# Performance work log

Measured on AMD Instinct MI355X. Metric: run time of the kernel, lower is better.

Reference implementation:

```python
import jax, jax.numpy as jnp
import numpy as np

B, S, D, H, W = 2, 4096, 1024, 8, 1024  # batch, seq, model_dim, heads, window
DH = D // H
EPS = 1e-5


def setup_inputs() -> dict:
    key = jax.random.key(0)
    ks = jax.random.split(key, 4)
    scale = 0.02
    return {
        "val": jax.random.normal(ks[0], (B, S, D), dtype=jnp.float32),
        "w_qkv": jax.random.normal(ks[1], (D, 3 * D), dtype=jnp.float32) * scale,
        "b_qkv": jnp.zeros((3 * D,), dtype=jnp.float32),
        "w_out": jax.random.normal(ks[2], (D, D), dtype=jnp.float32) * scale,
        "b_out": jnp.zeros((D,), dtype=jnp.float32),
        "ln_gamma": jnp.ones((D,), dtype=jnp.float32),
        "ln_beta": jnp.zeros((D,), dtype=jnp.float32),
    }


def _layer_norm(x, gamma, beta):
    mu = jnp.mean(x, axis=-1, keepdims=True)
    var = jnp.mean(jnp.square(x - mu), axis=-1, keepdims=True)
    return (x - mu) * jax.lax.rsqrt(var + EPS) * gamma + beta


def reference(val, w_qkv, b_qkv, w_out, b_out, ln_gamma, ln_beta):
    nb = S // W  # number of local windows
    qkv = val @ w_qkv + b_qkv                       # [B, S, 3D]
    qkv = qkv.reshape(B, nb, W, 3, H, DH)
    q, k, v = qkv[..., 0, :, :], qkv[..., 1, :, :], qkv[..., 2, :, :]  # [B,nb,W,H,DH]
    scores = jnp.einsum("bnwhd,bnxhd->bnhwx", q, k) / jnp.sqrt(jnp.float32(DH))
    attn = jax.nn.softmax(scores, axis=-1)          # [B,nb,H,W,W]
    ctx = jnp.einsum("bnhwx,bnxhd->bnwhd", attn, v).reshape(B, S, D)
    attn_out = ctx @ w_out + b_out                  # [B,S,D]
    return _layer_norm(val + attn_out, ln_gamma, ln_beta)
```

## Files before the change

kernel.cpp:

```cpp
#include <hip/hip_runtime.h>
#include <hip/hip_bf16.h>
#include <stdint.h>


typedef float f32x4 __attribute__((ext_vector_type(4)));
typedef __bf16 bf16x8 __attribute__((ext_vector_type(8)));

static __device__ __forceinline__ unsigned short f2bf(float f) {
    unsigned int u = __builtin_bit_cast(unsigned int, f);
    u += 0x7fffu + ((u >> 16) & 1u);
    return (unsigned short)(u >> 16);
}

static __device__ __forceinline__ unsigned cvt_pk_bf16(float lo, float hi) {
    unsigned r;
    asm("v_cvt_pk_bf16_f32 %0, %1, %2" : "=v"(r) : "v"(lo), "v"(hi));
    return r;
}

static __device__ __forceinline__ void gload_lds16(const void* g, void* l) {
    __builtin_amdgcn_global_load_lds(
        (__attribute__((address_space(1))) void*)(g),
        (__attribute__((address_space(3))) void*)(l), 16, 0, 0);
}

#define VMCNT(n) asm volatile("s_waitcnt vmcnt(" #n ")" ::: "memory")
#define SB() __builtin_amdgcn_sched_barrier(0)

__global__ __launch_bounds__(256) void k_convert(const float* __restrict__ in,
                                                 unsigned short* __restrict__ out,
                                                 int n4) {
    int i = blockIdx.x * 256 + threadIdx.x;
    if (i >= n4) return;
    float4 v = ((const float4*)in)[i];
    ushort4 o;
    o.x = f2bf(v.x); o.y = f2bf(v.y); o.z = f2bf(v.z); o.w = f2bf(v.w);
    ((ushort4*)out)[i] = o;
}

__global__ __launch_bounds__(256) void k_transpose(const float* __restrict__ in,
                                                   unsigned short* __restrict__ out,
                                                   int R, int C) {
    __shared__ float tile[64][65];
    const int rt = blockIdx.y * 64, ct = blockIdx.x * 64;
    const int t = threadIdx.x;
#pragma unroll
    for (int i = 0; i < 4; ++i) {
        int fid = i * 256 + t;
        int r = fid >> 4;
        int c = (fid & 15) << 2;
        float4 v = *(const float4*)&in[(size_t)(rt + r) * C + ct + c];
        tile[r][c] = v.x; tile[r][c + 1] = v.y; tile[r][c + 2] = v.z; tile[r][c + 3] = v.w;
    }
    __syncthreads();
#pragma unroll
    for (int i = 0; i < 4; ++i) {
        int fid = i * 256 + t;
        int c = fid >> 4;
        int r0 = (fid & 15) << 2;
        ushort4 o;
        o.x = f2bf(tile[r0][c]);     o.y = f2bf(tile[r0 + 1][c]);
        o.z = f2bf(tile[r0 + 2][c]); o.w = f2bf(tile[r0 + 3][c]);
        *(ushort4*)&out[(size_t)(ct + c) * R + rt + r0] = o;
    }
}

template <int MODE, int NTILES>
__global__ __launch_bounds__(512) void k_gemm(
    const unsigned short* __restrict__ A,
    const unsigned short* __restrict__ Bt,
    const float* __restrict__ bias,
    const float* __restrict__ resid,
    unsigned short* __restrict__ out_qk,
    unsigned short* __restrict__ out_vT,
    float* __restrict__ out_f)
{
    __shared__ __align__(16) char smem[147456];
    const int t = threadIdx.x;
    const int wave = t >> 6, lane = t & 63;
    const int lr = lane & 15, lg = lane >> 4;
    const int wr = wave >> 1, wc = wave & 1;

    const int lid = blockIdx.x;
    const int swz = (lid & 7) * (4 * NTILES) + (lid >> 3);
    const int tile_m = (swz / NTILES) * 256;
    const int tile_n = (swz % NTILES) * 128;

    const int srow = lane >> 3;
    const int sblk = (lane & 7) ^ srow;

    f32x4 acc[4][4];
#pragma unroll
    for (int i = 0; i < 4; ++i)
#pragma unroll
        for (int j = 0; j < 4; ++j)
            acc[i][j] = (f32x4){0.f, 0.f, 0.f, 0.f};

    auto stage2 = [&](int kt, int buf, int h) {
#pragma unroll
        for (int i = 0; i < 2; ++i) {
            int r = h * 128 + i * 64 + wave * 8 + srow;
            int dst = buf * 49152 + h * 16384 + i * 8192 + wave * 1024 + lane * 16;
            gload_lds16(&A[(size_t)(tile_m + r) * 1024 + kt * 64 + sblk * 8], smem + dst);
        }
        int rb = h * 64 + wave * 8 + srow;
        int dstb = buf * 49152 + 32768 + h * 8192 + wave * 1024 + lane * 16;
        gload_lds16(&Bt[(size_t)(tile_n + rb) * 1024 + kt * 64 + sblk * 8], smem + dstb);
    };

    stage2(0, 0, 0); stage2(0, 0, 1);
    stage2(1, 1, 0); stage2(1, 1, 1);

    bf16x8 af[4][2], bf[2][2];

    for (int kt = 0; kt < 16; ++kt) {
        const int buf = kt % 3;
        if (kt == 15) { VMCNT(0); } else { VMCNT(6); }
        SB(); __builtin_amdgcn_s_barrier(); SB();

        if (kt < 14) {
            stage2(kt + 2, (kt + 2) % 3, 0);
            stage2(kt + 2, (kt + 2) % 3, 1);
        }

        const int abase = buf * 49152;
        const int bbase = buf * 49152 + 32768;

#pragma unroll
        for (int mi = 0; mi < 4; ++mi) {
            const int row = wr * 64 + mi * 16 + lr;
#pragma unroll
            for (int kk = 0; kk < 2; ++kk)
                af[mi][kk] = *(const bf16x8*)(smem + abase + row * 128 +
                                (((kk * 4 + lg) ^ (row & 7)) << 4));
        }
#pragma unroll
        for (int ni = 0; ni < 2; ++ni) {
            const int row = wc * 64 + ni * 16 + lr;
#pragma unroll
            for (int kk = 0; kk < 2; ++kk)
                bf[ni][kk] = *(const bf16x8*)(smem + bbase + row * 128 +
                                (((kk * 4 + lg) ^ (row & 7)) << 4));
        }

        __builtin_amdgcn_s_setprio(1);
#pragma unroll
        for (int kk = 0; kk < 2; ++kk)
#pragma unroll
            for (int mi = 0; mi < 4; ++mi)
#pragma unroll
                for (int ni = 0; ni < 2; ++ni)
                    acc[mi][ni] = __builtin_amdgcn_mfma_f32_16x16x32_bf16(
                        af[mi][kk], bf[ni][kk], acc[mi][ni], 0, 0, 0);
        __builtin_amdgcn_s_setprio(0);

#pragma unroll
        for (int ni = 0; ni < 2; ++ni) {
            const int row = wc * 64 + 32 + ni * 16 + lr;
#pragma unroll
            for (int kk = 0; kk < 2; ++kk)
                bf[ni][kk] = *(const bf16x8*)(smem + bbase + row * 128 +
                                (((kk * 4 + lg) ^ (row & 7)) << 4));
        }

        __builtin_amdgcn_s_setprio(1);
#pragma unroll
        for (int kk = 0; kk < 2; ++kk)
#pragma unroll
            for (int mi = 0; mi < 4; ++mi)
#pragma unroll
                for (int ni = 0; ni < 2; ++ni)
                    acc[mi][2 + ni] = __builtin_amdgcn_mfma_f32_16x16x32_bf16(
                        af[mi][kk], bf[ni][kk], acc[mi][2 + ni], 0, 0, 0);
        __builtin_amdgcn_s_setprio(0);
    }

#pragma unroll
    for (int J = 0; J < 4; ++J) {
        const int n = tile_n + wc * 64 + J * 16 + lr;
        const float bv = bias[n];
#pragma unroll
        for (int I = 0; I < 4; ++I) {
            const int m0 = tile_m + wr * 64 + I * 16 + lg * 4;
            f32x4 v = acc[I][J];
            if (MODE == 0) {
                if (n < 2048) {
#pragma unroll
                    for (int r = 0; r < 4; ++r)
                        out_qk[(size_t)(m0 + r) * 2048 + n] = f2bf(v[r] + bv);
                } else {
                    int hd = (n - 2048) >> 7;
                    int dd = (n - 2048) & 127;
                    int bn = m0 >> 10;
                    int x0 = m0 & 1023;
                    ushort4 o;
                    o.x = f2bf(v[0] + bv); o.y = f2bf(v[1] + bv);
                    o.z = f2bf(v[2] + bv); o.w = f2bf(v[3] + bv);
                    *(ushort4*)&out_vT[((size_t)(bn * 8 + hd) * 128 + dd) * 1024 + x0] = o;
                }
            } else {
#pragma unroll
                for (int r = 0; r < 4; ++r) {
                    size_t idx = (size_t)(m0 + r) * 1024 + n;
                    out_f[idx] = v[r] + bv + resid[idx];
                }
            }
        }
    }
}

__global__ __launch_bounds__(256, 2) void k_attn(
    const unsigned short* __restrict__ qk,
    const unsigned short* __restrict__ vT,
    unsigned short* __restrict__ ctx)
{
    __shared__ __align__(16) unsigned short Kl[2 * 64 * 128];
    __shared__ __align__(16) unsigned short Vl[2 * 128 * 64];
    __shared__ __align__(16) unsigned short Pl[128 * 64];
    const int t = threadIdx.x;
    const int wave = t >> 6, lane = t & 63;
    const int lr = lane & 15, lg = lane >> 4;

    const int lid = blockIdx.y * gridDim.x + blockIdx.x;
    const int xcd = lid & 7, slot = lid >> 3;
    const int head = xcd * 8 + (slot & 7);
    const int qblk = slot >> 3;

    const int h = head & 7;
    const int tok0 = (head >> 3) * 1024;
    const int qtok = tok0 + qblk * 128 + wave * 32;
    const float cl2 = 0.08838834764831845f * 1.44269504088896f;

    const unsigned short* kbase = &qk[(size_t)tok0 * 2048 + 1024 + h * 128];
    const unsigned short* vhead = &vT[(size_t)head * 128 * 1024];

    auto stage = [&](int x0, int buf) {
        unsigned short* Kb = (unsigned short*)((char*)Kl + buf * 16384);
        unsigned short* Vb = (unsigned short*)((char*)Vl + buf * 16384);
#pragma unroll
        for (int i = 0; i < 4; ++i) {
            int x = i * 16 + wave * 4 + (lane >> 4);
            int ck = (lane & 15) ^ (x & 7);
            gload_lds16(&kbase[(size_t)(x0 + x) * 2048 + ck * 8], &Kb[i * 2048 + wave * 512]);
            int d = i * 32 + wave * 8 + (lane >> 3);
            int cv = (lane & 7) ^ (d & 7);
            gload_lds16(&vhead[(size_t)d * 1024 + x0 + cv * 8], &Vb[i * 2048 + wave * 512]);
        }
    };

    bf16x8 qf[2][4];
#pragma unroll
    for (int nq = 0; nq < 2; ++nq)
#pragma unroll
        for (int kk = 0; kk < 4; ++kk)
            qf[nq][kk] = *(const bf16x8*)&qk[(size_t)(qtok + 16 * nq + lr) * 2048 + h * 128 + kk * 32 + lg * 8];

    f32x4 o[2][8];
#pragma unroll
    for (int a = 0; a < 2; ++a)
#pragma unroll
        for (int b = 0; b < 8; ++b)
            o[a][b] = (f32x4){0.f, 0.f, 0.f, 0.f};
    float m_run[2] = {-3.0e38f, -3.0e38f};
    float l_run[2] = {0.f, 0.f};

    stage(0, 0);

    for (int tile = 0; tile < 16; ++tile) {
        const int kb = (tile & 1) * 16384;
        if (tile < 15) {
            stage((tile + 1) * 64, (tile + 1) & 1);
            VMCNT(8);
        } else {
            VMCNT(0);
        }
        SB(); __builtin_amdgcn_s_barrier(); SB();

        f32x4 s[4][2];
#pragma unroll
        for (int mi = 0; mi < 4; ++mi)
#pragma unroll
            for (int nq = 0; nq < 2; ++nq)
                s[mi][nq] = (f32x4){0.f, 0.f, 0.f, 0.f};
#pragma unroll
        for (int kk = 0; kk < 4; ++kk) {
            bf16x8 kf[4];
#pragma unroll
            for (int mi = 0; mi < 4; ++mi) {
                int row = mi * 16 + lr;
                int byte = (row * 256 + kk * 64 + lg * 16) ^ ((row & 7) << 4);
                kf[mi] = *(const bf16x8*)((const char*)Kl + kb + byte);
            }
            __builtin_amdgcn_s_setprio(1);
#pragma unroll
            for (int mi = 0; mi < 4; ++mi)
#pragma unroll
                for (int nq = 0; nq < 2; ++nq)
                    s[mi][nq] = __builtin_amdgcn_mfma_f32_16x16x32_bf16(kf[mi], qf[nq][kk], s[mi][nq], 0, 0, 0);
            __builtin_amdgcn_s_setprio(0);
        }

        float fac[2];
        bool doresc[2];
#pragma unroll
        for (int nq = 0; nq < 2; ++nq) {
            float mx = -3.0e38f;
#pragma unroll
            for (int mi = 0; mi < 4; ++mi)
#pragma unroll
                for (int r = 0; r < 4; ++r)
                    mx = fmaxf(mx, s[mi][nq][r]);
            mx = fmaxf(mx, __shfl_xor(mx, 16));
            mx = fmaxf(mx, __shfl_xor(mx, 32));
            float mxl = mx * cl2;
            float mr = m_run[nq];
            if (__any(mxl - mr > 8.0f)) {
                float mn = fmaxf(mr, mxl);
                fac[nq] = __builtin_amdgcn_exp2f(mr - mn);
                m_run[nq] = mn;
                doresc[nq] = true;
            } else {
                fac[nq] = 1.0f;
                doresc[nq] = false;
            }
            const float nmn = -m_run[nq];
            float sum = 0.f;
            const int q = wave * 32 + nq * 16 + lr;
#pragma unroll
            for (int mi = 0; mi < 4; ++mi) {
                float p0 = __builtin_amdgcn_exp2f(__builtin_fmaf(s[mi][nq][0], cl2, nmn));
                float p1 = __builtin_amdgcn_exp2f(__builtin_fmaf(s[mi][nq][1], cl2, nmn));
                float p2 = __builtin_amdgcn_exp2f(__builtin_fmaf(s[mi][nq][2], cl2, nmn));
                float p3 = __builtin_amdgcn_exp2f(__builtin_fmaf(s[mi][nq][3], cl2, nmn));
                sum += (p0 + p1) + (p2 + p3);
                uint2 pk;
                pk.x = cvt_pk_bf16(p0, p1);
                pk.y = cvt_pk_bf16(p2, p3);
                int byte = (q * 128 + (mi * 16 + lg * 4) * 2) ^ ((q & 7) << 4);
                *(uint2*)((char*)Pl + byte) = pk;
            }
            sum += __shfl_xor(sum, 16);
            sum += __shfl_xor(sum, 32);
            l_run[nq] = l_run[nq] * fac[nq] + sum;
        }

#pragma unroll
        for (int mo = 0; mo < 2; ++mo)
            if (doresc[mo]) {
#pragma unroll
                for (int r = 0; r < 4; ++r) {
                    int src = (lane & 48) | (lg * 4 + r);
                    float f = __shfl(fac[mo], src);
#pragma unroll
                    for (int nd = 0; nd < 8; ++nd)
                        o[mo][nd][r] *= f;
                }
            }

#pragma unroll
        for (int kk = 0; kk < 2; ++kk) {
            bf16x8 pf[2], vf[8];
#pragma unroll
            for (int mo = 0; mo < 2; ++mo) {
                int q = wave * 32 + mo * 16 + lr;
                int byte = (q * 128 + kk * 64 + lg * 16) ^ ((q & 7) << 4);
                pf[mo] = *(const bf16x8*)((const char*)Pl + byte);
            }
#pragma unroll
            for (int nd = 0; nd < 8; ++nd) {
                int drow = nd * 16 + lr;
                int byte = (drow * 128 + kk * 64 + lg * 16) ^ ((drow & 7) << 4);
                vf[nd] = *(const bf16x8*)((const char*)Vl + kb + byte);
            }
            __builtin_amdgcn_s_setprio(1);
#pragma unroll
            for (int mo = 0; mo < 2; ++mo)
#pragma unroll
                for (int nd = 0; nd < 8; ++nd)
                    o[mo][nd] = __builtin_amdgcn_mfma_f32_16x16x32_bf16(pf[mo], vf[nd], o[mo][nd], 0, 0, 0);
            __builtin_amdgcn_s_setprio(0);
        }
        __builtin_amdgcn_s_barrier(); SB();
    }

#pragma unroll
    for (int mo = 0; mo < 2; ++mo) {
        float rl[4];
#pragma unroll
        for (int r = 0; r < 4; ++r) {
            int src = (lane & 48) | (lg * 4 + r);
            rl[r] = 1.0f / __shfl(l_run[mo], src);
        }
#pragma unroll
        for (int nd = 0; nd < 8; ++nd)
#pragma unroll
            for (int r = 0; r < 4; ++r) {
                int q = qtok + mo * 16 + lg * 4 + r;
                ctx[(size_t)q * 1024 + h * 128 + nd * 16 + lr] = f2bf(o[mo][nd][r] * rl[r]);
            }
    }
}

__global__ __launch_bounds__(256) void k_ln(float* __restrict__ io,
                                            const float* __restrict__ gamma,
                                            const float* __restrict__ beta)
{
    __shared__ float bs[4], bss[4];
    const int row = blockIdx.x;
    const int t = threadIdx.x;
    float4 v = ((const float4*)&io[(size_t)row * 1024])[t];
    float s = (v.x + v.y) + (v.z + v.w);
    float ss = (v.x * v.x + v.y * v.y) + (v.z * v.z + v.w * v.w);
#pragma unroll
    for (int off = 32; off >= 1; off >>= 1) {
        s += __shfl_xor(s, off);
        ss += __shfl_xor(ss, off);
    }
    if ((t & 63) == 0) { bs[t >> 6] = s; bss[t >> 6] = ss; }
    __syncthreads();
    s = (bs[0] + bs[1]) + (bs[2] + bs[3]);
    ss = (bss[0] + bss[1]) + (bss[2] + bss[3]);
    const float mu = s * (1.f / 1024.f);
    const float var = ss * (1.f / 1024.f) - mu * mu;
    const float rs = rsqrtf(var + 1e-5f);
    float4 g = ((const float4*)gamma)[t];
    float4 b = ((const float4*)beta)[t];
    float4 ov;
    ov.x = (v.x - mu) * rs * g.x + b.x;
    ov.y = (v.y - mu) * rs * g.y + b.y;
    ov.z = (v.z - mu) * rs * g.z + b.z;
    ov.w = (v.w - mu) * rs * g.w + b.w;
    ((float4*)&io[(size_t)row * 1024])[t] = ov;
}

extern "C" void kernel_launch(void* const* d_in, const int* in_sizes, int n_in,
                              void* d_out, int out_size, void* d_ws, size_t ws_size,
                              hipStream_t stream)
{
    const float* val   = (const float*)d_in[0];
    const float* w_qkv = (const float*)d_in[1];
    const float* b_qkv = (const float*)d_in[2];
    const float* w_out = (const float*)d_in[3];
    const float* b_out = (const float*)d_in[4];
    const float* ln_g  = (const float*)d_in[5];
    const float* ln_b  = (const float*)d_in[6];
    float* out = (float*)d_out;

    char* ws = (char*)d_ws;
    unsigned short* qk     = (unsigned short*)(ws + 0);
    unsigned short* vTb    = (unsigned short*)(ws + 33554432);
    unsigned short* ctx    = (unsigned short*)(ws + 50331648);
    unsigned short* w_outT = (unsigned short*)(ws + 67108864);
    unsigned short* w_qkvT = (unsigned short*)(ws + 69206016);
    unsigned short* valb   = (unsigned short*)(ws + 75497472);

    k_convert<<<8192, 256, 0, stream>>>(val, valb, 2097152);
    k_transpose<<<dim3(48, 16), 256, 0, stream>>>(w_qkv, w_qkvT, 1024, 3072);
    k_transpose<<<dim3(16, 16), 256, 0, stream>>>(w_out, w_outT, 1024, 1024);
    k_gemm<0, 24><<<768, 512, 0, stream>>>(valb, w_qkvT, b_qkv, nullptr, qk, vTb, nullptr);
    k_attn<<<dim3(8, 64), 256, 0, stream>>>(qk, vTb, ctx);
    k_gemm<1, 8><<<256, 512, 0, stream>>>(ctx, w_outT, b_out, val, nullptr, nullptr, out);
    k_ln<<<8192, 256, 0, stream>>>(out, ln_g, ln_b);
}
```

Before: 159.5 us.

## Halve GEMM block to 4 waves with 128x64 per-wave tiles

Rewrites the GEMM work split so each block runs 4 waves instead of 8, and each wave computes a 128x64 output sub-tile with 32 accumulators. Each wave now issues all of its staging loads and reuses A/B fragments across more MFMAs per LDS read, which cuts the number of LDS reads per MFMA. In exchange it roughly doubles accumulator register pressure (128 VGPRs for accumulators) and leaves fewer waves to hide latency.

```diff
diff --git a/kernel.cpp b/kernel.cpp
--- a/kernel.cpp
+++ b/kernel.cpp
@@ -66,7 +66,7 @@
 }
 
 template <int MODE, int NTILES>
-__global__ __launch_bounds__(512) void k_gemm(
+__global__ __launch_bounds__(256) void k_gemm(
     const unsigned short* __restrict__ A,
     const unsigned short* __restrict__ Bt,
     const float* __restrict__ bias,
@@ -89,90 +89,66 @@
     const int srow = lane >> 3;
     const int sblk = (lane & 7) ^ srow;
 
-    f32x4 acc[4][4];
-#pragma unroll
-    for (int i = 0; i < 4; ++i)
+    f32x4 acc[8][4];
+#pragma unroll
+    for (int i = 0; i < 8; ++i)
 #pragma unroll
         for (int j = 0; j < 4; ++j)
             acc[i][j] = (f32x4){0.f, 0.f, 0.f, 0.f};
 
-    auto stage2 = [&](int kt, int buf, int h) {
-#pragma unroll
-        for (int i = 0; i < 2; ++i) {
-            int r = h * 128 + i * 64 + wave * 8 + srow;
-            int dst = buf * 49152 + h * 16384 + i * 8192 + wave * 1024 + lane * 16;
+    auto stage = [&](int kt, int buf) {
+#pragma unroll
+        for (int i = 0; i < 8; ++i) {
+            int r = wave * 64 + i * 8 + srow;
+            int dst = buf * 49152 + wave * 8192 + i * 1024 + lane * 16;
             gload_lds16(&A[(size_t)(tile_m + r) * 1024 + kt * 64 + sblk * 8], smem + dst);
         }
-        int rb = h * 64 + wave * 8 + srow;
-        int dstb = buf * 49152 + 32768 + h * 8192 + wave * 1024 + lane * 16;
-        gload_lds16(&Bt[(size_t)(tile_n + rb) * 1024 + kt * 64 + sblk * 8], smem + dstb);
+#pragma unroll
+        for (int i = 0; i < 4; ++i) {
+            int r = wave * 32 + i * 8 + srow;
+            int dst = buf * 49152 + 32768 + wave * 4096 + i * 1024 + lane * 16;
+            gload_lds16(&Bt[(size_t)(tile_n + r) * 1024 + kt * 64 + sblk * 8], smem + dst);
+        }
     };
 
-    stage2(0, 0, 0); stage2(0, 0, 1);
-    stage2(1, 1, 0); stage2(1, 1, 1);
-
-    bf16x8 af[4][2], bf[2][2];
+    stage(0, 0);
+    stage(1, 1);
+
+    bf16x8 af[8], bf[4];
 
     for (int kt = 0; kt < 16; ++kt) {
         const int buf = kt % 3;
-        if (kt == 15) { VMCNT(0); } else { VMCNT(6); }
+        if (kt == 15) { VMCNT(0); } else { VMCNT(12); }
         SB(); __builtin_amdgcn_s_barrier(); SB();
 
-        if (kt < 14) {
-            stage2(kt + 2, (kt + 2) % 3, 0);
-            stage2(kt + 2, (kt + 2) % 3, 1);
-        }
+        if (kt < 14) stage(kt + 2, (kt + 2) % 3);
 
         const int abase = buf * 49152;
         const int bbase = buf * 49152 + 32768;
 
 #pragma unroll
-        for (int mi = 0; mi < 4; ++mi) {
-            const int row = wr * 64 + mi * 16 + lr;
-#pragma unroll
-            for (int kk = 0; kk < 2; ++kk)
-                af[mi][kk] = *(const bf16x8*)(smem + abase + row * 128 +
+        for (int kk = 0; kk < 2; ++kk) {
+#pragma unroll
+            for (int mi = 0; mi < 8; ++mi) {
+                const int row = wr * 128 + mi * 16 + lr;
+                af[mi] = *(const bf16x8*)(smem + abase + row * 128 +
                                 (((kk * 4 + lg) ^ (row & 7)) << 4));
-        }
-#pragma unroll
-        for (int ni = 0; ni < 2; ++ni) {
-            const int row = wc * 64 + ni * 16 + lr;
-#pragma unroll
-            for (int kk = 0; kk < 2; ++kk)
-                bf[ni][kk] = *(const bf16x8*)(smem + bbase + row * 128 +
+            }
+#pragma unroll
+            for (int ni = 0; ni < 4; ++ni) {
+                const int row = wc * 64 + ni * 16 + lr;
+                bf[ni] = *(const bf16x8*)(smem + bbase + row * 128 +
                                 (((kk * 4 + lg) ^ (row & 7)) << 4));
-        }
-
-        __builtin_amdgcn_s_setprio(1);
-#pragma unroll
-        for (int kk = 0; kk < 2; ++kk)
-#pragma unroll
-            for (int mi = 0; mi < 4; ++mi)
-#pragma unroll
-                for (int ni = 0; ni < 2; ++ni)
+            }
+            __builtin_amdgcn_s_setprio(1);
+#pragma unroll
+            for (int mi = 0; mi < 8; ++mi)
+#pragma unroll
+                for (int ni = 0; ni < 4; ++ni)
                     acc[mi][ni] = __builtin_amdgcn_mfma_f32_16x16x32_bf16(
-                        af[mi][kk], bf[ni][kk], acc[mi][ni], 0, 0, 0);
-        __builtin_amdgcn_s_setprio(0);
-
-#pragma unroll
-        for (int ni = 0; ni < 2; ++ni) {
-            const int row = wc * 64 + 32 + ni * 16 + lr;
-#pragma unroll
-            for (int kk = 0; kk < 2; ++kk)
-                bf[ni][kk] = *(const bf16x8*)(smem + bbase + row * 128 +
-                                (((kk * 4 + lg) ^ (row & 7)) << 4));
-        }
-
-        __builtin_amdgcn_s_setprio(1);
-#pragma unroll
-        for (int kk = 0; kk < 2; ++kk)
-#pragma unroll
-            for (int mi = 0; mi < 4; ++mi)
-#pragma unroll
-                for (int ni = 0; ni < 2; ++ni)
-                    acc[mi][2 + ni] = __builtin_amdgcn_mfma_f32_16x16x32_bf16(
-                        af[mi][kk], bf[ni][kk], acc[mi][2 + ni], 0, 0, 0);
-        __builtin_amdgcn_s_setprio(0);
+                        af[mi], bf[ni], acc[mi][ni], 0, 0, 0);
+            __builtin_amdgcn_s_setprio(0);
+        }
     }
 
 #pragma unroll
@@ -180,8 +156,8 @@
         const int n = tile_n + wc * 64 + J * 16 + lr;
         const float bv = bias[n];
 #pragma unroll
-        for (int I = 0; I < 4; ++I) {
-            const int m0 = tile_m + wr * 64 + I * 16 + lg * 4;
+        for (int I = 0; I < 8; ++I) {
+            const int m0 = tile_m + wr * 128 + I * 16 + lg * 4;
             f32x4 v = acc[I][J];
             if (MODE == 0) {
                 if (n < 2048) {
@@ -457,8 +433,8 @@
     k_convert<<<8192, 256, 0, stream>>>(val, valb, 2097152);
     k_transpose<<<dim3(48, 16), 256, 0, stream>>>(w_qkv, w_qkvT, 1024, 3072);
     k_transpose<<<dim3(16, 16), 256, 0, stream>>>(w_out, w_outT, 1024, 1024);
-    k_gemm<0, 24><<<768, 512, 0, stream>>>(valb, w_qkvT, b_qkv, nullptr, qk, vTb, nullptr);
+    k_gemm<0, 24><<<768, 256, 0, stream>>>(valb, w_qkvT, b_qkv, nullptr, qk, vTb, nullptr);
     k_attn<<<dim3(8, 64), 256, 0, stream>>>(qk, vTb, ctx);
-    k_gemm<1, 8><<<256, 512, 0, stream>>>(ctx, w_outT, b_out, val, nullptr, nullptr, out);
+    k_gemm<1, 8><<<256, 256, 0, stream>>>(ctx, w_outT, b_out, val, nullptr, nullptr, out);
     k_ln<<<8192, 256, 0, stream>>>(out, ln_g, ln_b);
 }
```

Result: slower. 173.4 us (+8.7%).
